# Kernel tuning notes

Measured on AMD Instinct MI355X. Metric: run time of the kernel, lower is better.

## Reference

```python
import jax, jax.numpy as jnp
import numpy as np

I = 1739   # input/output feature size (num_nodes)
H = 256    # hidden size
T = 2048   # trajectory length


def gru(x_seq, h0, W_ih, W_hh, b_ih, b_hh):
    """PyTorch-convention GRU over x_seq [T, I] with h0 [H]. Returns (hs [T,H], h_T [H])."""
    x_proj = x_seq @ W_ih.T + b_ih  # [T, 3H], precompute input projections

    def step(h, xp):
        hh = h @ W_hh.T + b_hh  # [3H]
        xr, xz, xn = xp[:H], xp[H:2 * H], xp[2 * H:]
        hr, hz, hn = hh[:H], hh[H:2 * H], hh[2 * H:]
        r = jax.nn.sigmoid(xr + hr)
        z = jax.nn.sigmoid(xz + hz)
        n = jnp.tanh(xn + r * hn)
        h_new = (1.0 - z) * n + z * h
        return h_new, h_new

    h_T, hs = jax.lax.scan(step, h0, x_proj)
    return hs, h_T


def setup_inputs() -> dict:
    key = jax.random.key(0)
    ks = jax.random.split(key, 12)
    s = 1.0 / np.sqrt(H)
    inp = {
        "input_trajectory": jax.random.normal(ks[0], (1, T, I), jnp.float32),
        "target_trajectory": jax.random.normal(ks[1], (1, T, I), jnp.float32),
        "W_ih_enc": jax.random.uniform(ks[2], (3 * H, I), jnp.float32, -s, s),
        "W_hh_enc": jax.random.uniform(ks[3], (3 * H, H), jnp.float32, -s, s),
        "b_ih_enc": jax.random.uniform(ks[4], (3 * H,), jnp.float32, -s, s),
        "b_hh_enc": jax.random.uniform(ks[5], (3 * H,), jnp.float32, -s, s),
        "W_ih_dec": jax.random.uniform(ks[6], (3 * H, I), jnp.float32, -s, s),
        "W_hh_dec": jax.random.uniform(ks[7], (3 * H, H), jnp.float32, -s, s),
        "b_ih_dec": jax.random.uniform(ks[8], (3 * H,), jnp.float32, -s, s),
        "b_hh_dec": jax.random.uniform(ks[9], (3 * H,), jnp.float32, -s, s),
        "W_out": jax.random.uniform(ks[10], (I, H), jnp.float32, -s, s),
        "b_out": jax.random.uniform(ks[11], (I,), jnp.float32, -s, s),
    }
    return inp


def reference(input_trajectory, target_trajectory,
              W_ih_enc, W_hh_enc, b_ih_enc, b_hh_enc,
              W_ih_dec, W_hh_dec, b_ih_dec, b_hh_dec,
              W_out, b_out):
    x = input_trajectory[0]  # [T, I], batch=1
    h0 = jnp.zeros((H,), x.dtype)
    # Encoder: only the final hidden state is used.
    _, h_enc = gru(x, h0, W_ih_enc, W_hh_enc, b_ih_enc, b_hh_enc)
    # Decoder: loop feeds each input timestep through a 1-step GRU;
    # this is exactly a GRU over the full sequence starting from h_enc.
    hs, _ = gru(x, h_enc, W_ih_dec, W_hh_dec, b_ih_dec, b_hh_dec)  # [T, H]
    # Per-step Linear is a single batched matmul over all steps.
    preds = hs @ W_out.T + b_out  # [T, I]
    # Original cats per-step (1,1,I) tensors along dim=0 -> [T, 1, I].
    return preds[:, None, :]
```

## Files before the change

kernel.cpp:

```cpp
#include <hip/hip_runtime.h>
#include <hip/hip_fp16.h>

#define TT 2048
#define II 1739
#define HN 256
#define H3 768

typedef _Float16 h2 __attribute__((ext_vector_type(2)));

__device__ __forceinline__ float fdot2(h2 a, h2 b, float c) {
  return __builtin_amdgcn_fdot2(a, b, c, false);
}

template <int CTRL>
__device__ __forceinline__ float dpp_qperm(float v) {
  int r = __builtin_amdgcn_update_dpp(0, __builtin_bit_cast(int, v), CTRL, 0xF, 0xF, true);
  return __builtin_bit_cast(float, r);
}

__global__ __launch_bounds__(256) void gemm_abt(
    const float* __restrict__ A, int M, int K,
    const float* __restrict__ B, int N,
    const float* __restrict__ bias1, const float* __restrict__ bias2, int b2lim,
    float* __restrict__ C) {
  __shared__ float As[16][64];
  __shared__ float Bs[16][64];
  const int tid = threadIdx.x;
  const int m0 = blockIdx.y * 64, n0 = blockIdx.x * 64;
  const int lr = tid >> 2;
  const int lk = (tid & 3) * 4;
  const int cx = tid & 15, cy = tid >> 4;
  float acc[4][4] = {};

  for (int k0 = 0; k0 < K; k0 += 16) {
#pragma unroll
    for (int i = 0; i < 4; ++i) {
      int k = k0 + lk + i;
      As[lk + i][lr] = (k < K) ? A[(size_t)(m0 + lr) * K + k] : 0.f;
      int bn = n0 + lr;
      Bs[lk + i][lr] = (k < K && bn < N) ? B[(size_t)bn * K + k] : 0.f;
    }
    __syncthreads();
#pragma unroll
    for (int k = 0; k < 16; ++k) {
      float4 av = *(const float4*)&As[k][cy * 4];
      float4 bv = *(const float4*)&Bs[k][cx * 4];
      const float aa[4] = {av.x, av.y, av.z, av.w};
      const float bb[4] = {bv.x, bv.y, bv.z, bv.w};
#pragma unroll
      for (int i = 0; i < 4; ++i)
#pragma unroll
        for (int j = 0; j < 4; ++j) acc[i][j] = fmaf(aa[i], bb[j], acc[i][j]);
    }
    __syncthreads();
  }
#pragma unroll
  for (int i = 0; i < 4; ++i) {
    int m = m0 + cy * 4 + i;
#pragma unroll
    for (int j = 0; j < 4; ++j) {
      int n = n0 + cx * 4 + j;
      if (n < N) {
        float b = bias1 ? bias1[n] : 0.f;
        if (bias2 && n < b2lim) b += bias2[n];
        C[(size_t)m * N + n] = acc[i][j] + b;
      }
    }
  }
}

__global__ __launch_bounds__(512) __attribute__((amdgpu_waves_per_eu(2, 2)))
void gru_seq(
    const float* __restrict__ xp,
    const float* __restrict__ Whh,
    const float* __restrict__ bhh,
    const float* __restrict__ h0,
    float* __restrict__ hs_out,
    float* __restrict__ hT_out) {
  __shared__ uint4 hbuf[4 * 9];
  __shared__ float hh[H3];

  const int tid = threadIdx.x;
  const int lane = tid & 63;
  const int wv = tid >> 6;
  const int kc = lane & 3;
  const int g = wv * 16 + (lane >> 2);
  const int r0 = g * 6;

  h2 wreg[6][32];
#pragma unroll
  for (int i = 0; i < 6; ++i) {
    const float* wr = Whh + (size_t)(r0 + i) * HN + kc * 64;
#pragma unroll
    for (int p = 0; p < 32; ++p) {
      float2 f = *(const float2*)(wr + 2 * p);
      wreg[i][p] = h2{(_Float16)f.x, (_Float16)f.y};
    }
  }

  float hj = 0.f, bhn = 0.f;
  if (tid < HN) {
    hj = h0 ? h0[tid] : 0.f;
    bhn = bhh[2 * HN + tid];
    ((_Float16*)hbuf)[(tid >> 6) * 72 + (tid & 63)] = (_Float16)hj;
  }
  __syncthreads();

  float xr = 0.f, xz = 0.f, xn = 0.f;
  if (tid < HN) {
    const float* xpt = xp + tid;
    xr = xpt[0];
    xz = xpt[HN];
    xn = xpt[2 * HN];
  }

  for (int t = 0; t < TT; ++t) {
    float nxr = 0.f, nxz = 0.f, nxn = 0.f;
    if (tid < HN && t + 1 < TT) {
      const float* xpt = xp + (size_t)(t + 1) * H3 + tid;
      nxr = xpt[0];
      nxz = xpt[HN];
      nxn = xpt[2 * HN];
    }

    uint4 hv[8];
#pragma unroll
    for (int j = 0; j < 8; ++j) hv[j] = hbuf[kc * 9 + j];

    float acc[6] = {0.f, 0.f, 0.f, 0.f, 0.f, 0.f};
#pragma unroll
    for (int hf = 0; hf < 2; ++hf) {
#pragma unroll
      for (int i = 0; i < 6; ++i) {
#pragma unroll
        for (int p = 0; p < 16; ++p) {
          uint d = ((const uint*)&hv[hf * 4 + (p >> 2)])[p & 3];
          acc[i] = fdot2(wreg[i][hf * 16 + p], __builtin_bit_cast(h2, d), acc[i]);
        }
      }
    }

#pragma unroll
    for (int i = 0; i < 6; ++i) {
      float v = acc[i];
      v += dpp_qperm<0xB1>(v);
      v += dpp_qperm<0x4E>(v);
      acc[i] = v;
    }
    if (kc == 0) {
      *(float2*)&hh[r0 + 0] = make_float2(acc[0], acc[1]);
      *(float2*)&hh[r0 + 2] = make_float2(acc[2], acc[3]);
      *(float2*)&hh[r0 + 4] = make_float2(acc[4], acc[5]);
    }
    __syncthreads();

    if (tid < HN) {
      float r = 1.f / (1.f + __expf(-(xr + hh[tid])));
      float z = 1.f / (1.f + __expf(-(xz + hh[HN + tid])));
      float nv = 2.f / (1.f + __expf(-2.f * (xn + r * (hh[2 * HN + tid] + bhn)))) - 1.f;
      hj = (1.f - z) * nv + z * hj;
      if (hs_out) hs_out[(size_t)t * HN + tid] = hj;
      ((_Float16*)hbuf)[(tid >> 6) * 72 + (tid & 63)] = (_Float16)hj;
    }
    xr = nxr; xz = nxz; xn = nxn;
    __syncthreads();
  }
  if (hT_out && tid < HN) hT_out[tid] = hj;
}

extern "C" void kernel_launch(void* const* d_in, const int* in_sizes, int n_in,
                              void* d_out, int out_size, void* d_ws, size_t ws_size,
                              hipStream_t stream) {
  const float* x     = (const float*)d_in[0];
  const float* Wih_e = (const float*)d_in[2];
  const float* Whh_e = (const float*)d_in[3];
  const float* bih_e = (const float*)d_in[4];
  const float* bhh_e = (const float*)d_in[5];
  const float* Wih_d = (const float*)d_in[6];
  const float* Whh_d = (const float*)d_in[7];
  const float* bih_d = (const float*)d_in[8];
  const float* bhh_d = (const float*)d_in[9];
  const float* Wout  = (const float*)d_in[10];
  const float* bout  = (const float*)d_in[11];
  float* out = (float*)d_out;

  float* ws = (float*)d_ws;
  float* xpe  = ws;
  float* xpd  = xpe + (size_t)TT * H3;
  float* hs   = xpd + (size_t)TT * H3;
  float* henc = hs + (size_t)TT * HN;

  dim3 blk(256);
  gemm_abt<<<dim3(12, 32), blk, 0, stream>>>(x, TT, II, Wih_e, H3, bih_e, bhh_e, 2 * HN, xpe);
  gemm_abt<<<dim3(12, 32), blk, 0, stream>>>(x, TT, II, Wih_d, H3, bih_d, bhh_d, 2 * HN, xpd);
  gru_seq<<<1, 512, 0, stream>>>(xpe, Whh_e, bhh_e, nullptr, nullptr, henc);
  gru_seq<<<1, 512, 0, stream>>>(xpd, Whh_d, bhh_d, henc, hs, nullptr);
  gemm_abt<<<dim3(28, 32), blk, 0, stream>>>(hs, TT, HN, Wout, II, bout, nullptr, 0, out);
}
```

Baseline: 5.679 ms.

## Compute GRU recurrent matvec with MFMA 16x16x32 f16 instead of fdot2

The per-step W_hh·h product in the GRU recurrence moves from per-lane fdot2 chains to MFMA 16x16x32 f16 instructions. Weight fragments are preloaded into registers in the MFMA A layout. The hidden vector is broadcast across all 16 B columns, so column 0 of each output tile holds the result. This removes the DPP quad reductions and the padded shared-memory layout. In exchange it wastes 15/16 of the MFMA columns and adds MFMA issue latency to the serial critical path of every timestep.

```diff
diff --git a/kernel.cpp b/kernel.cpp
--- a/kernel.cpp
+++ b/kernel.cpp
@@ -6,17 +6,8 @@
 #define HN 256
 #define H3 768
 
-typedef _Float16 h2 __attribute__((ext_vector_type(2)));
-
-__device__ __forceinline__ float fdot2(h2 a, h2 b, float c) {
-  return __builtin_amdgcn_fdot2(a, b, c, false);
-}
-
-template <int CTRL>
-__device__ __forceinline__ float dpp_qperm(float v) {
-  int r = __builtin_amdgcn_update_dpp(0, __builtin_bit_cast(int, v), CTRL, 0xF, 0xF, true);
-  return __builtin_bit_cast(float, r);
-}
+typedef _Float16 h8v __attribute__((ext_vector_type(8)));
+typedef float f4v __attribute__((ext_vector_type(4)));
 
 __global__ __launch_bounds__(256) void gemm_abt(
     const float* __restrict__ A, int M, int K,
@@ -77,24 +68,26 @@
     const float* __restrict__ h0,
     float* __restrict__ hs_out,
     float* __restrict__ hT_out) {
-  __shared__ uint4 hbuf[4 * 9];
+  __shared__ _Float16 hbuf[HN];
   __shared__ float hh[H3];
 
   const int tid = threadIdx.x;
   const int lane = tid & 63;
   const int wv = tid >> 6;
-  const int kc = lane & 3;
-  const int g = wv * 16 + (lane >> 2);
-  const int r0 = g * 6;
+  const int q = lane >> 4;
+  const int ml = lane & 15;
 
-  h2 wreg[6][32];
+  h8v afrag[6][8];
 #pragma unroll
   for (int i = 0; i < 6; ++i) {
-    const float* wr = Whh + (size_t)(r0 + i) * HN + kc * 64;
+    const float* wr = Whh + (size_t)(96 * wv + 16 * i + ml) * HN + 8 * q;
 #pragma unroll
-    for (int p = 0; p < 32; ++p) {
-      float2 f = *(const float2*)(wr + 2 * p);
-      wreg[i][p] = h2{(_Float16)f.x, (_Float16)f.y};
+    for (int kc = 0; kc < 8; ++kc) {
+      const float* wp = wr + 32 * kc;
+      float4 a = *(const float4*)wp;
+      float4 b = *(const float4*)(wp + 4);
+      afrag[i][kc] = h8v{(_Float16)a.x, (_Float16)a.y, (_Float16)a.z, (_Float16)a.w,
+                         (_Float16)b.x, (_Float16)b.y, (_Float16)b.z, (_Float16)b.w};
     }
   }
 
@@ -102,7 +95,7 @@
   if (tid < HN) {
     hj = h0 ? h0[tid] : 0.f;
     bhn = bhh[2 * HN + tid];
-    ((_Float16*)hbuf)[(tid >> 6) * 72 + (tid & 63)] = (_Float16)hj;
+    hbuf[tid] = (_Float16)hj;
   }
   __syncthreads();
 
@@ -123,34 +116,28 @@
       nxn = xpt[2 * HN];
     }
 
-    uint4 hv[8];
+    f4v acc[6];
 #pragma unroll
-    for (int j = 0; j < 8; ++j) hv[j] = hbuf[kc * 9 + j];
+    for (int i = 0; i < 6; ++i) acc[i] = f4v{0.f, 0.f, 0.f, 0.f};
 
-    float acc[6] = {0.f, 0.f, 0.f, 0.f, 0.f, 0.f};
 #pragma unroll
-    for (int hf = 0; hf < 2; ++hf) {
+    for (int ph = 0; ph < 2; ++ph) {
+      h8v hv[4];
 #pragma unroll
-      for (int i = 0; i < 6; ++i) {
+      for (int c = 0; c < 4; ++c)
+        hv[c] = *(const h8v*)((const char*)hbuf + 64 * (ph * 4 + c) + 16 * q);
 #pragma unroll
-        for (int p = 0; p < 16; ++p) {
-          uint d = ((const uint*)&hv[hf * 4 + (p >> 2)])[p & 3];
-          acc[i] = fdot2(wreg[i][hf * 16 + p], __builtin_bit_cast(h2, d), acc[i]);
-        }
+      for (int c = 0; c < 4; ++c) {
+#pragma unroll
+        for (int i = 0; i < 6; ++i)
+          acc[i] = __builtin_amdgcn_mfma_f32_16x16x32_f16(afrag[i][ph * 4 + c], hv[c], acc[i], 0, 0, 0);
       }
     }
 
+    if (ml == 0) {
 #pragma unroll
-    for (int i = 0; i < 6; ++i) {
-      float v = acc[i];
-      v += dpp_qperm<0xB1>(v);
-      v += dpp_qperm<0x4E>(v);
-      acc[i] = v;
-    }
-    if (kc == 0) {
-      *(float2*)&hh[r0 + 0] = make_float2(acc[0], acc[1]);
-      *(float2*)&hh[r0 + 2] = make_float2(acc[2], acc[3]);
-      *(float2*)&hh[r0 + 4] = make_float2(acc[4], acc[5]);
+      for (int i = 0; i < 6; ++i)
+        *(f4v*)(hh + 96 * wv + 16 * i + 4 * q) = acc[i];
     }
     __syncthreads();
 
@@ -160,7 +147,7 @@
       float nv = 2.f / (1.f + __expf(-2.f * (xn + r * (hh[2 * HN + tid] + bhn)))) - 1.f;
       hj = (1.f - z) * nv + z * hj;
       if (hs_out) hs_out[(size_t)t * HN + tid] = hj;
-      ((_Float16*)hbuf)[(tid >> 6) * 72 + (tid & 63)] = (_Float16)hj;
+      hbuf[tid] = (_Float16)hj;
     }
     xr = nxr; xz = nxz; xn = nxn;
     __syncthreads();
```

Measured after the change: 6.146 ms. 8.2% more time.

## Assign gate rows per thread group so GRU step needs one barrier

Applied to the files above, without the earlier changes.

Each 4-lane group now owns the r, z and n rows for the same two hidden units, so the gate math runs right after the DPP reduction, with no shared-memory exchange of the hh vector. The hidden state buffer is double-buffered, which removes one of the two block barriers per timestep; the remaining barrier is written as inline asm. The h vector is now read from LDS in uint4 chunks inside the dot loop instead of being preloaded into registers. The trade-off is that gate work is spread over 128 lanes across all waves, and correctness relies on the hand-written waitcnt/barrier sequence.

```diff
diff --git a/kernel.cpp b/kernel.cpp
--- a/kernel.cpp
+++ b/kernel.cpp
@@ -77,67 +77,75 @@
     const float* __restrict__ h0,
     float* __restrict__ hs_out,
     float* __restrict__ hT_out) {
-  __shared__ uint4 hbuf[4 * 9];
-  __shared__ float hh[H3];
+  __shared__ uint hbuf[2][144];
 
   const int tid = threadIdx.x;
-  const int lane = tid & 63;
-  const int wv = tid >> 6;
-  const int kc = lane & 3;
-  const int g = wv * 16 + (lane >> 2);
-  const int r0 = g * 6;
-
+  const int p = tid >> 2;
+  const int kc = tid & 3;
+  const int u0 = 2 * p;
+  const bool gl = (kc == 0);
+
+  int rows[6];
+  rows[0] = u0;          rows[1] = u0 + 1;
+  rows[2] = 256 + u0;    rows[3] = 256 + u0 + 1;
+  rows[4] = 512 + u0;    rows[5] = 512 + u0 + 1;
   h2 wreg[6][32];
 #pragma unroll
   for (int i = 0; i < 6; ++i) {
-    const float* wr = Whh + (size_t)(r0 + i) * HN + kc * 64;
-#pragma unroll
-    for (int p = 0; p < 32; ++p) {
-      float2 f = *(const float2*)(wr + 2 * p);
-      wreg[i][p] = h2{(_Float16)f.x, (_Float16)f.y};
-    }
-  }
-
-  float hj = 0.f, bhn = 0.f;
-  if (tid < HN) {
-    hj = h0 ? h0[tid] : 0.f;
-    bhn = bhh[2 * HN + tid];
-    ((_Float16*)hbuf)[(tid >> 6) * 72 + (tid & 63)] = (_Float16)hj;
+    const float* wr = Whh + (size_t)rows[i] * HN + kc * 64;
+#pragma unroll
+    for (int c = 0; c < 8; ++c) {
+      float4 a = *(const float4*)(wr + 8 * c);
+      float4 b = *(const float4*)(wr + 8 * c + 4);
+      wreg[i][4 * c + 0] = h2{(_Float16)a.x, (_Float16)a.y};
+      wreg[i][4 * c + 1] = h2{(_Float16)a.z, (_Float16)a.w};
+      wreg[i][4 * c + 2] = h2{(_Float16)b.x, (_Float16)b.y};
+      wreg[i][4 * c + 3] = h2{(_Float16)b.z, (_Float16)b.w};
+    }
+  }
+
+  float hj0 = 0.f, hj1 = 0.f, bhn0 = 0.f, bhn1 = 0.f;
+  const int ch = p >> 5;
+  const int eh = p & 31;
+  if (gl) {
+    if (h0) { float2 h = *(const float2*)(h0 + u0); hj0 = h.x; hj1 = h.y; }
+    float2 b = *(const float2*)(bhh + 2 * HN + u0);
+    bhn0 = b.x; bhn1 = b.y;
+    h2 hp = h2{(_Float16)hj0, (_Float16)hj1};
+    hbuf[0][36 * ch + eh] = __builtin_bit_cast(uint, hp);
   }
   __syncthreads();
 
-  float xr = 0.f, xz = 0.f, xn = 0.f;
-  if (tid < HN) {
-    const float* xpt = xp + tid;
-    xr = xpt[0];
-    xz = xpt[HN];
-    xn = xpt[2 * HN];
+  float xr0 = 0, xr1 = 0, xz0 = 0, xz1 = 0, xn0 = 0, xn1 = 0;
+  if (gl) {
+    float2 a = *(const float2*)(xp + u0);
+    float2 b = *(const float2*)(xp + HN + u0);
+    float2 c = *(const float2*)(xp + 2 * HN + u0);
+    xr0 = a.x; xr1 = a.y; xz0 = b.x; xz1 = b.y; xn0 = c.x; xn1 = c.y;
   }
 
   for (int t = 0; t < TT; ++t) {
-    float nxr = 0.f, nxz = 0.f, nxn = 0.f;
-    if (tid < HN && t + 1 < TT) {
-      const float* xpt = xp + (size_t)(t + 1) * H3 + tid;
-      nxr = xpt[0];
-      nxz = xpt[HN];
-      nxn = xpt[2 * HN];
-    }
-
-    uint4 hv[8];
-#pragma unroll
-    for (int j = 0; j < 8; ++j) hv[j] = hbuf[kc * 9 + j];
+    float nr0 = 0, nr1 = 0, nz0 = 0, nz1 = 0, nn0 = 0, nn1 = 0;
+    if (gl && t + 1 < TT) {
+      const float* xpt = xp + (size_t)(t + 1) * H3;
+      float2 a = *(const float2*)(xpt + u0);
+      float2 b = *(const float2*)(xpt + HN + u0);
+      float2 c = *(const float2*)(xpt + 2 * HN + u0);
+      nr0 = a.x; nr1 = a.y; nz0 = b.x; nz1 = b.y; nn0 = c.x; nn1 = c.y;
+    }
+
+    const uint* hb = hbuf[t & 1] + 36 * kc;
 
     float acc[6] = {0.f, 0.f, 0.f, 0.f, 0.f, 0.f};
 #pragma unroll
-    for (int hf = 0; hf < 2; ++hf) {
-#pragma unroll
-      for (int i = 0; i < 6; ++i) {
-#pragma unroll
-        for (int p = 0; p < 16; ++p) {
-          uint d = ((const uint*)&hv[hf * 4 + (p >> 2)])[p & 3];
-          acc[i] = fdot2(wreg[i][hf * 16 + p], __builtin_bit_cast(h2, d), acc[i]);
-        }
-      }
+    for (int c = 0; c < 8; ++c) {
+      uint4 hv = *(const uint4*)(hb + 4 * c);
+      const uint hw[4] = {hv.x, hv.y, hv.z, hv.w};
+#pragma unroll
+      for (int i = 0; i < 6; ++i)
+#pragma unroll
+        for (int j = 0; j < 4; ++j)
+          acc[i] = fdot2(wreg[i][4 * c + j], __builtin_bit_cast(h2, hw[j]), acc[i]);
     }
 
 #pragma unroll
@@ -147,25 +155,24 @@
       v += dpp_qperm<0x4E>(v);
       acc[i] = v;
     }
-    if (kc == 0) {
-      *(float2*)&hh[r0 + 0] = make_float2(acc[0], acc[1]);
-      *(float2*)&hh[r0 + 2] = make_float2(acc[2], acc[3]);
-      *(float2*)&hh[r0 + 4] = make_float2(acc[4], acc[5]);
-    }
-    __syncthreads();
-
-    if (tid < HN) {
-      float r = 1.f / (1.f + __expf(-(xr + hh[tid])));
-      float z = 1.f / (1.f + __expf(-(xz + hh[HN + tid])));
-      float nv = 2.f / (1.f + __expf(-2.f * (xn + r * (hh[2 * HN + tid] + bhn)))) - 1.f;
-      hj = (1.f - z) * nv + z * hj;
-      if (hs_out) hs_out[(size_t)t * HN + tid] = hj;
-      ((_Float16*)hbuf)[(tid >> 6) * 72 + (tid & 63)] = (_Float16)hj;
-    }
-    xr = nxr; xz = nxz; xn = nxn;
-    __syncthreads();
-  }
-  if (hT_out && tid < HN) hT_out[tid] = hj;
+
+    if (gl) {
+      float r0 = 1.f / (1.f + __expf(-(xr0 + acc[0])));
+      float r1 = 1.f / (1.f + __expf(-(xr1 + acc[1])));
+      float z0 = 1.f / (1.f + __expf(-(xz0 + acc[2])));
+      float z1 = 1.f / (1.f + __expf(-(xz1 + acc[3])));
+      float n0 = 2.f / (1.f + __expf(-2.f * (xn0 + r0 * (acc[4] + bhn0)))) - 1.f;
+      float n1 = 2.f / (1.f + __expf(-2.f * (xn1 + r1 * (acc[5] + bhn1)))) - 1.f;
+      hj0 = (1.f - z0) * n0 + z0 * hj0;
+      hj1 = (1.f - z1) * n1 + z1 * hj1;
+      if (hs_out) *(float2*)(hs_out + (size_t)t * HN + u0) = make_float2(hj0, hj1);
+      h2 hp = h2{(_Float16)hj0, (_Float16)hj1};
+      hbuf[(t + 1) & 1][36 * ch + eh] = __builtin_bit_cast(uint, hp);
+    }
+    xr0 = nr0; xr1 = nr1; xz0 = nz0; xz1 = nz1; xn0 = nn0; xn1 = nn1;
+    asm volatile("s_waitcnt lgkmcnt(0)\n\ts_barrier" ::: "memory");
+  }
+  if (hT_out && gl) *(float2*)(hT_out + u0) = make_float2(hj0, hj1);
 }
 
 extern "C" void kernel_launch(void* const* d_in, const int* in_sizes, int n_in,
```

Measured after the change: 6.272 ms. 10.4% more time.
